# Kernel tuning notes

Measured on AMD Instinct MI355X. Metric: run time of the kernel, lower is better.

Reference implementation:

```python
import jax, jax.numpy as jnp
import numpy as np

N_NODES = 100000
N_EDGES = 1600000
IN_FEATS = 128
HID = 128
OUT_FEATS = 64


def setup_inputs() -> dict:
    key = jax.random.key(0)
    ks = jax.random.split(key, 8)
    node_ids = jnp.arange(N_NODES, dtype=jnp.int64)
    src = jax.random.randint(ks[0], (N_EDGES,), 0, N_NODES, dtype=jnp.int64)
    dst = jax.random.randint(ks[1], (N_EDGES,), 0, N_NODES, dtype=jnp.int64)
    emb = jax.random.normal(ks[2], (N_NODES, IN_FEATS), dtype=jnp.float32)
    W1 = jax.random.normal(ks[3], (IN_FEATS, HID), dtype=jnp.float32) / np.sqrt(IN_FEATS)
    b1 = jnp.zeros((HID,), dtype=jnp.float32)
    W2 = jax.random.normal(ks[4], (HID, OUT_FEATS), dtype=jnp.float32) / np.sqrt(HID)
    b2 = jnp.zeros((OUT_FEATS,), dtype=jnp.float32)
    return {"node_ids": node_ids, "src": src, "dst": dst, "emb": emb,
            "W1": W1, "b1": b1, "W2": W2, "b2": b2}


def _sym_norms(src, dst):
    # DGL GraphConv norm='both': D_out^{-1/2} on source side, D_in^{-1/2} on dest side,
    # degrees clamped to >= 1.
    ones = jnp.ones(src.shape[0], dtype=jnp.float32)
    deg_out = jax.ops.segment_sum(ones, src, num_segments=N_NODES)
    deg_in = jax.ops.segment_sum(ones, dst, num_segments=N_NODES)
    norm_src = jnp.clip(deg_out, 1.0, None) ** -0.5  # [N]
    norm_dst = jnp.clip(deg_in, 1.0, None) ** -0.5   # [N]
    return norm_src, norm_dst


def _spmm(src, dst, h):
    # rst[dst] += h[src]  (sparse adjacency aggregation)
    return jax.ops.segment_sum(h[src], dst, num_segments=N_NODES)


def reference(node_ids, src, dst, emb, W1, b1, W2, b2):
    norm_src, norm_dst = _sym_norms(src, dst)
    h = emb[node_ids]                                   # [N, IN]
    # Layer 1 (IN -> HID, relu): weight applied after aggregation (in <= out)
    h = _spmm(src, dst, h * norm_src[:, None]) * norm_dst[:, None]
    h = jax.nn.relu(h @ W1 + b1)                        # [N, HID]
    # Dropout(0.5) is identity in eval mode.
    # Layer 2 (HID -> OUT): DGL applies weight BEFORE aggregation when in > out
    h = (h @ W2) * norm_src[:, None]                    # [N, OUT]
    h = _spmm(src, dst, h) * norm_dst[:, None] + b2
    return h
```

## Files before the change

### kernel.cpp

```cpp
#include <hip/hip_runtime.h>

#define N_N 100000
#define N_E 1600000
#define SLOTS 48
#define N_PAD 100096

#define BK_SHIFT 9
#define BK_SIZE 512
#define NBKT 196
#define MAXB 10240
#define EPB2 4096
#define NBLK2 ((N_E + EPB2 - 1) / EPB2)
#define EPT 16

#define BINC_BLKS (2 * NBKT)
#define EMB_BLKS 3125
#define W_BLKS 48

typedef unsigned short ushort_t;
typedef unsigned int uint_t;
typedef _Float16 f16x8 __attribute__((ext_vector_type(8)));
typedef float f32x4 __attribute__((ext_vector_type(4)));

__device__ __forceinline__ ushort_t f2h(float f) {
    union { _Float16 h; ushort_t u; } c; c.h = (_Float16)f; return c.u;
}

__device__ __forceinline__ void acc2h(uint_t v, float wv, float& a, float& b) {
    union { uint_t u; _Float16 h[2]; } c; c.u = v;
    a = fmaf((float)c.h[0], wv, a);
    b = fmaf((float)c.h[1], wv, b);
}

__device__ __forceinline__ void addh(uint_t v, float& a, float& b) {
    union { uint_t u; _Float16 h[2]; } c; c.u = v;
    a += (float)c.h[0];
    b += (float)c.h[1];
}

__global__ void __launch_bounds__(256) k_scatter(
        const int* __restrict__ src, const int* __restrict__ dst,
        int* __restrict__ cur_d, int* __restrict__ cur_s,
        uint_t* __restrict__ pe_dst, uint_t* __restrict__ pe_src) {
    __shared__ int hd[NBKT], hs[NBKT], od[NBKT], os_[NBKT];
    int t = threadIdx.x, blk = blockIdx.x;
    for (int i = t; i < NBKT; i += 256) { hd[i] = 0; hs[i] = 0; }
    __syncthreads();
    int e0 = blk * EPB2;
    int myS[EPT], myD[EPT];
    uint_t myR[EPT];
#pragma unroll
    for (int i = 0; i < EPT; i++) {
        int e = e0 + t + i * 256;
        if (e < N_E) {
            int s = src[e], d = dst[e];
            myS[i] = s; myD[i] = d;
            uint_t rd = (uint_t)atomicAdd(&hd[d >> BK_SHIFT], 1);
            uint_t rs = (uint_t)atomicAdd(&hs[s >> BK_SHIFT], 1);
            myR[i] = rd | (rs << 16);
        }
    }
    __syncthreads();
    for (int i = t; i < NBKT; i += 256) {
        int c = hd[i]; od[i]  = c ? atomicAdd(&cur_d[i], c) : 0;
        c = hs[i];     os_[i] = c ? atomicAdd(&cur_s[i], c) : 0;
    }
    __syncthreads();
#pragma unroll
    for (int i = 0; i < EPT; i++) {
        int e = e0 + t + i * 256;
        if (e < N_E) {
            int s = myS[i], d = myD[i];
            int rd = od[d >> BK_SHIFT] + (int)(myR[i] & 0xffffu);
            int rs = os_[s >> BK_SHIFT] + (int)(myR[i] >> 16);
            if (rd < MAXB) pe_dst[(size_t)(d >> BK_SHIFT) * MAXB + rd] =
                               (uint_t)s | ((uint_t)(d & 511) << 17);
            if (rs < MAXB) pe_src[(size_t)(s >> BK_SHIFT) * MAXB + rs] = (uint_t)s;
        }
    }
}

__global__ void __launch_bounds__(512) k_binC_prep(
        const uint_t* __restrict__ pe_dst, const uint_t* __restrict__ pe_src,
        const int* __restrict__ cur_d, const int* __restrict__ cur_s,
        int* __restrict__ slots, int* __restrict__ cnt,
        float* __restrict__ nd, float* __restrict__ ns,
        const float* __restrict__ emb, ushort_t* __restrict__ embf,
        const float* __restrict__ W1, const float* __restrict__ W2,
        ushort_t* __restrict__ w1f, ushort_t* __restrict__ w2f) {
    int t = threadIdx.x, bb = blockIdx.x;
    if (bb >= BINC_BLKS) {
        int pb = bb - BINC_BLKS;
        if (pb < EMB_BLKS) {
            int i = pb * 1024 + t;
            const float4* E4 = (const float4*)emb;
            ushort4* O4 = (ushort4*)embf;
            float4 v0 = E4[i], v1 = E4[i + 512];
            ushort4 o0, o1;
            o0.x = f2h(v0.x); o0.y = f2h(v0.y); o0.z = f2h(v0.z); o0.w = f2h(v0.w);
            o1.x = f2h(v1.x); o1.y = f2h(v1.y); o1.z = f2h(v1.z); o1.w = f2h(v1.w);
            O4[i] = o0; O4[i + 512] = o1;
        } else {
            int idx = (pb - EMB_BLKS) * 512 + t;
            int j = idx & 7, l = (idx >> 3) & 63;
            int k = (l >> 4) * 8 + j;
            int n = l & 15;
            if (idx < 16384) {
                int kc = (idx >> 9) & 3, nt = idx >> 11;
                w1f[idx] = f2h(W1[(kc * 32 + k) * 128 + nt * 16 + n]);
            } else {
                int i2 = idx - 16384;
                int kc = (i2 >> 9) & 3, nt = i2 >> 11;
                w2f[i2] = f2h(W2[(kc * 32 + k) * 64 + nt * 16 + n]);
            }
        }
        return;
    }
    __shared__ int lc[BK_SIZE];
    for (int i = t; i < BK_SIZE; i += 512) lc[i] = 0;
    __syncthreads();
    if (bb < NBKT) {
        int b = bb;
        int cb = min(cur_d[b], MAXB);
        int nbase = b << BK_SHIFT;
        const uint_t* pe = pe_dst + (size_t)b * MAXB;
        for (int e = t; e < cb; e += 512) {
            uint_t ed = pe[e];
            int dloc = (int)(ed >> 17);
            int s = (int)(ed & 0x1ffffu);
            int pos = atomicAdd(&lc[dloc], 1);
            if (pos < SLOTS) slots[(size_t)(nbase + dloc) * SLOTS + pos] = s;
        }
        __syncthreads();
        for (int i = t; i < BK_SIZE; i += 512) {
            int n = nbase + i;
            if (n < N_N) {
                int c = lc[i];
                cnt[n] = c;
                nd[n] = 1.0f / sqrtf((float)max(c, 1));
            }
        }
    } else {
        int b = bb - NBKT;
        int cb = min(cur_s[b], MAXB);
        int nbase = b << BK_SHIFT;
        const uint_t* pe = pe_src + (size_t)b * MAXB;
        for (int e = t; e < cb; e += 512)
            atomicAdd(&lc[(int)pe[e] - nbase], 1);
        __syncthreads();
        for (int i = t; i < BK_SIZE; i += 512) {
            int n = nbase + i;
            if (n < N_N) ns[n] = 1.0f / sqrtf((float)max(lc[i], 1));
        }
    }
}

__global__ void __launch_bounds__(256) k_spmm1(
        const int* __restrict__ cnt, const int* __restrict__ slots,
        const ushort_t* __restrict__ embf, const float* __restrict__ ns,
        const float* __restrict__ nd, uint_t* __restrict__ aggf) {
    int wid = (blockIdx.x * 256 + (int)threadIdx.x) >> 6;
    int node = __builtin_amdgcn_readfirstlane(wid);
    if (node >= N_N) return;
    int lane = threadIdx.x & 63;
    const int* row = slots + node * SLOTS;
    int len = min(cnt[node], SLOTS);
    float ax0 = 0.f, ay0 = 0.f, ax1 = 0.f, ay1 = 0.f;
    int e = 0;
    int n8 = len & ~7;
    for (; e < n8; e += 8) {
        int s0 = __builtin_amdgcn_readfirstlane(row[e + 0]);
        int s1 = __builtin_amdgcn_readfirstlane(row[e + 1]);
        int s2 = __builtin_amdgcn_readfirstlane(row[e + 2]);
        int s3 = __builtin_amdgcn_readfirstlane(row[e + 3]);
        int s4 = __builtin_amdgcn_readfirstlane(row[e + 4]);
        int s5 = __builtin_amdgcn_readfirstlane(row[e + 5]);
        int s6 = __builtin_amdgcn_readfirstlane(row[e + 6]);
        int s7 = __builtin_amdgcn_readfirstlane(row[e + 7]);
        float w0 = ns[s0], w1 = ns[s1], w2 = ns[s2], w3 = ns[s3];
        float w4 = ns[s4], w5 = ns[s5], w6 = ns[s6], w7 = ns[s7];
        uint_t v0 = ((const uint_t*)(embf + (size_t)s0 * 128))[lane];
        uint_t v1 = ((const uint_t*)(embf + (size_t)s1 * 128))[lane];
        uint_t v2 = ((const uint_t*)(embf + (size_t)s2 * 128))[lane];
        uint_t v3 = ((const uint_t*)(embf + (size_t)s3 * 128))[lane];
        uint_t v4 = ((const uint_t*)(embf + (size_t)s4 * 128))[lane];
        uint_t v5 = ((const uint_t*)(embf + (size_t)s5 * 128))[lane];
        uint_t v6 = ((const uint_t*)(embf + (size_t)s6 * 128))[lane];
        uint_t v7 = ((const uint_t*)(embf + (size_t)s7 * 128))[lane];
        acc2h(v0, w0, ax0, ay0);
        acc2h(v1, w1, ax1, ay1);
        acc2h(v2, w2, ax0, ay0);
        acc2h(v3, w3, ax1, ay1);
        acc2h(v4, w4, ax0, ay0);
        acc2h(v5, w5, ax1, ay1);
        acc2h(v6, w6, ax0, ay0);
        acc2h(v7, w7, ax1, ay1);
    }
    int n4 = len & ~3;
    for (; e < n4; e += 4) {
        int s0 = __builtin_amdgcn_readfirstlane(row[e + 0]);
        int s1 = __builtin_amdgcn_readfirstlane(row[e + 1]);
        int s2 = __builtin_amdgcn_readfirstlane(row[e + 2]);
        int s3 = __builtin_amdgcn_readfirstlane(row[e + 3]);
        float w0 = ns[s0], w1 = ns[s1], w2 = ns[s2], w3 = ns[s3];
        uint_t v0 = ((const uint_t*)(embf + (size_t)s0 * 128))[lane];
        uint_t v1 = ((const uint_t*)(embf + (size_t)s1 * 128))[lane];
        uint_t v2 = ((const uint_t*)(embf + (size_t)s2 * 128))[lane];
        uint_t v3 = ((const uint_t*)(embf + (size_t)s3 * 128))[lane];
        acc2h(v0, w0, ax0, ay0);
        acc2h(v1, w1, ax1, ay1);
        acc2h(v2, w2, ax0, ay0);
        acc2h(v3, w3, ax1, ay1);
    }
    for (; e < len; ++e) {
        int s = __builtin_amdgcn_readfirstlane(row[e]);
        float w = ns[s];
        uint_t v = ((const uint_t*)(embf + (size_t)s * 128))[lane];
        acc2h(v, w, ax0, ay0);
    }
    float sc = nd[node];
    union { _Float16 h[2]; uint_t u; } p;
    p.h[0] = (_Float16)((ax0 + ax1) * sc);
    p.h[1] = (_Float16)((ay0 + ay1) * sc);
    aggf[(size_t)node * 64 + lane] = p.u;
}

#define HSTH 136
__global__ void __launch_bounds__(256, 2) k_gemm(
        const ushort_t* __restrict__ aggf, const ushort_t* __restrict__ w1f,
        const float* __restrict__ b1, const ushort_t* __restrict__ w2f,
        const float* __restrict__ ns, ushort_t* __restrict__ h2b) {
    __shared__ ushort_t sh[128 * HSTH];
    int t = threadIdx.x;
    int w = t >> 6, l = t & 63;
    int quad = l >> 4, lm = l & 15;
    int nb0 = blockIdx.x * 128;

    f16x8 a[2][4];
#pragma unroll
    for (int rt = 0; rt < 2; rt++)
#pragma unroll
        for (int kc = 0; kc < 4; kc++)
            a[rt][kc] = *(const f16x8*)(aggf
                + (size_t)(nb0 + rt * 64 + w * 16 + lm) * 128 + kc * 32 + quad * 8);

    f32x4 acc[2][8];
#pragma unroll
    for (int rt = 0; rt < 2; rt++)
#pragma unroll
        for (int nt = 0; nt < 8; nt++) acc[rt][nt] = (f32x4){0.f, 0.f, 0.f, 0.f};

#pragma unroll
    for (int kc = 0; kc < 4; kc++) {
        f16x8 bq[8];
#pragma unroll
        for (int nt = 0; nt < 8; nt++)
            bq[nt] = *(const f16x8*)(w1f + (((nt * 4 + kc) * 64 + l) << 3));
#pragma unroll
        for (int nt = 0; nt < 8; nt++) {
            acc[0][nt] = __builtin_amdgcn_mfma_f32_16x16x32_f16(a[0][kc], bq[nt], acc[0][nt], 0, 0, 0);
            acc[1][nt] = __builtin_amdgcn_mfma_f32_16x16x32_f16(a[1][kc], bq[nt], acc[1][nt], 0, 0, 0);
        }
    }
#pragma unroll
    for (int nt = 0; nt < 8; nt++) {
        float bb = b1[nt * 16 + lm];
#pragma unroll
        for (int rt = 0; rt < 2; rt++)
#pragma unroll
            for (int r = 0; r < 4; r++) {
                int row = rt * 64 + w * 16 + quad * 4 + r;
                sh[row * HSTH + nt * 16 + lm] = f2h(fmaxf(acc[rt][nt][r] + bb, 0.f));
            }
    }
    __syncthreads();

    f16x8 h[2][4];
#pragma unroll
    for (int rt = 0; rt < 2; rt++)
#pragma unroll
        for (int kc = 0; kc < 4; kc++)
            h[rt][kc] = *(const f16x8*)(sh + (rt * 64 + w * 16 + lm) * HSTH
                                        + kc * 32 + quad * 8);

    f32x4 acc2[2][4];
#pragma unroll
    for (int rt = 0; rt < 2; rt++)
#pragma unroll
        for (int q = 0; q < 4; q++) acc2[rt][q] = (f32x4){0.f, 0.f, 0.f, 0.f};

#pragma unroll
    for (int kc = 0; kc < 4; kc++) {
        f16x8 b2q[4];
#pragma unroll
        for (int q = 0; q < 4; q++)
            b2q[q] = *(const f16x8*)(w2f + (((q * 4 + kc) * 64 + l) << 3));
#pragma unroll
        for (int q = 0; q < 4; q++) {
            acc2[0][q] = __builtin_amdgcn_mfma_f32_16x16x32_f16(h[0][kc], b2q[q], acc2[0][q], 0, 0, 0);
            acc2[1][q] = __builtin_amdgcn_mfma_f32_16x16x32_f16(h[1][kc], b2q[q], acc2[1][q], 0, 0, 0);
        }
    }
#pragma unroll
    for (int rt = 0; rt < 2; rt++)
#pragma unroll
        for (int r = 0; r < 4; r++) {
            int node = nb0 + rt * 64 + w * 16 + quad * 4 + r;
            if (node < N_N) {
                float s = ns[node];
#pragma unroll
                for (int q = 0; q < 4; q++)
                    h2b[(size_t)node * 64 + q * 16 + lm] = f2h(acc2[rt][q][r] * s);
            }
        }
}

__global__ void __launch_bounds__(256) k_spmm2(
        const int* __restrict__ cnt, const int* __restrict__ slots,
        const ushort_t* __restrict__ h2b, const float* __restrict__ nd,
        const float* __restrict__ b2, float* __restrict__ out) {
    int wid = (blockIdx.x * 256 + (int)threadIdx.x) >> 6;
    int node = __builtin_amdgcn_readfirstlane(wid);
    if (node >= N_N) return;
    int lane = threadIdx.x & 63;
    int half = lane >> 5, w32 = lane & 31;
    const int* row = slots + node * SLOTS;
    int len = min(cnt[node], SLOTS);
    const uint_t* H = (const uint_t*)h2b;
    float a0 = 0.f, a1 = 0.f, b0 = 0.f, b1v = 0.f;
    int e = 0;
    int n8 = len & ~7;
    for (; e < n8; e += 8) {
        int i0 = e + half;
        int s0 = row[i0], s1 = row[i0 + 2], s2 = row[i0 + 4], s3 = row[i0 + 6];
        uint_t v0 = H[(size_t)s0 * 32 + w32];
        uint_t v1 = H[(size_t)s1 * 32 + w32];
        uint_t v2 = H[(size_t)s2 * 32 + w32];
        uint_t v3 = H[(size_t)s3 * 32 + w32];
        addh(v0, a0, a1);
        addh(v1, b0, b1v);
        addh(v2, a0, a1);
        addh(v3, b0, b1v);
    }
    for (; e + 1 < len; e += 2) {
        int s = row[e + half];
        uint_t v = H[(size_t)s * 32 + w32];
        addh(v, a0, a1);
    }
    if (e < len && half == 0) {
        int s = row[e];
        uint_t v = H[(size_t)s * 32 + w32];
        addh(v, a0, a1);
    }
    a0 += b0; a1 += b1v;
    a0 += __shfl_xor(a0, 32);
    a1 += __shfl_xor(a1, 32);
    if (half == 0) {
        float sc = nd[node];
        float2 bb = ((const float2*)b2)[w32];
        float2 o;
        o.x = a0 * sc + bb.x;
        o.y = a1 * sc + bb.y;
        ((float2*)(out + (size_t)node * 64))[w32] = o;
    }
}

extern "C" void kernel_launch(void* const* d_in, const int* in_sizes, int n_in,
                              void* d_out, int out_size, void* d_ws, size_t ws_size,
                              hipStream_t stream) {
    const int* src = (const int*)d_in[1];
    const int* dst = (const int*)d_in[2];
    const float* emb = (const float*)d_in[3];
    const float* W1 = (const float*)d_in[4];
    const float* b1 = (const float*)d_in[5];
    const float* W2 = (const float*)d_in[6];
    const float* b2 = (const float*)d_in[7];
    float* out = (float*)d_out;

    int* cur_d   = (int*)d_ws;
    int* cur_s   = cur_d + 256;
    int* cnt     = cur_s + 256;
    float* ns    = (float*)(cnt + N_PAD);
    float* nd    = ns + N_PAD;
    int* slots   = (int*)(nd + N_PAD);
    uint_t* pe_dst = (uint_t*)(slots + (size_t)N_N * SLOTS);
    uint_t* pe_src = pe_dst + (size_t)NBKT * MAXB;
    ushort_t* embf = (ushort_t*)(pe_src + (size_t)NBKT * MAXB);
    uint_t* aggf = (uint_t*)(embf + (size_t)N_PAD * 128);
    ushort_t* w1f = (ushort_t*)(aggf + (size_t)N_PAD * 64);
    ushort_t* w2f = w1f + 16384;
    ushort_t* h2b = w2f + 8192;

    hipMemsetAsync(cur_d, 0, sizeof(int) * 512, stream);
    k_scatter  <<<NBLK2, 256, 0, stream>>>(src, dst, cur_d, cur_s, pe_dst, pe_src);
    k_binC_prep<<<BINC_BLKS + EMB_BLKS + W_BLKS, 512, 0, stream>>>(
        pe_dst, pe_src, cur_d, cur_s, slots, cnt, nd, ns, emb, embf, W1, W2, w1f, w2f);
    k_spmm1 <<<(N_N + 3) / 4, 256, 0, stream>>>(cnt, slots, embf, ns, nd, aggf);
    k_gemm  <<<N_PAD / 128, 256, 0, stream>>>((const ushort_t*)aggf, w1f, b1, w2f, ns, h2b);
    k_spmm2 <<<(N_N + 3) / 4, 256, 0, stream>>>(cnt, slots, h2b, nd, b2, out);
}
```

Baseline: 299.2 us.

## Count source degrees with global atomics and widen SpMM gathers to 8-byte loads

The source-side degree count no longer goes through a bucketed pe_src scatter plus a second binning pass. It now uses direct global atomicAdds into a per-node counter, which removes a large write and read buffer at the cost of 1.6M global atomics. Both SpMM kernels now split each wavefront across two or four edges at once, with each lane loading uint2 (8 bytes) instead of 4 bytes. Partial sums are combined with cross-lane shuffles, raising memory-level parallelism per wave. The memset grows to clear the per-node counter array.

```diff
diff --git a/kernel.cpp b/kernel.cpp
--- a/kernel.cpp
+++ b/kernel.cpp
@@ -38,32 +38,35 @@
     b += (float)c.h[1];
 }
 
+__device__ __forceinline__ uint_t packh2(float a, float b) {
+    union { _Float16 h[2]; uint_t u; } p;
+    p.h[0] = (_Float16)a; p.h[1] = (_Float16)b;
+    return p.u;
+}
+
 __global__ void __launch_bounds__(256) k_scatter(
         const int* __restrict__ src, const int* __restrict__ dst,
-        int* __restrict__ cur_d, int* __restrict__ cur_s,
-        uint_t* __restrict__ pe_dst, uint_t* __restrict__ pe_src) {
-    __shared__ int hd[NBKT], hs[NBKT], od[NBKT], os_[NBKT];
+        int* __restrict__ cur_d, int* __restrict__ cnt_s,
+        uint_t* __restrict__ pe_dst) {
+    __shared__ int hd[NBKT], od[NBKT];
     int t = threadIdx.x, blk = blockIdx.x;
-    for (int i = t; i < NBKT; i += 256) { hd[i] = 0; hs[i] = 0; }
+    for (int i = t; i < NBKT; i += 256) hd[i] = 0;
     __syncthreads();
     int e0 = blk * EPB2;
-    int myS[EPT], myD[EPT];
-    uint_t myR[EPT];
+    int myS[EPT], myD[EPT], myR[EPT];
 #pragma unroll
     for (int i = 0; i < EPT; i++) {
         int e = e0 + t + i * 256;
         if (e < N_E) {
             int s = src[e], d = dst[e];
             myS[i] = s; myD[i] = d;
-            uint_t rd = (uint_t)atomicAdd(&hd[d >> BK_SHIFT], 1);
-            uint_t rs = (uint_t)atomicAdd(&hs[s >> BK_SHIFT], 1);
-            myR[i] = rd | (rs << 16);
+            myR[i] = atomicAdd(&hd[d >> BK_SHIFT], 1);
+            atomicAdd(&cnt_s[s], 1);
         }
     }
     __syncthreads();
     for (int i = t; i < NBKT; i += 256) {
-        int c = hd[i]; od[i]  = c ? atomicAdd(&cur_d[i], c) : 0;
-        c = hs[i];     os_[i] = c ? atomicAdd(&cur_s[i], c) : 0;
+        int c = hd[i]; od[i] = c ? atomicAdd(&cur_d[i], c) : 0;
     }
     __syncthreads();
 #pragma unroll
@@ -71,18 +74,16 @@
         int e = e0 + t + i * 256;
         if (e < N_E) {
             int s = myS[i], d = myD[i];
-            int rd = od[d >> BK_SHIFT] + (int)(myR[i] & 0xffffu);
-            int rs = os_[s >> BK_SHIFT] + (int)(myR[i] >> 16);
+            int rd = od[d >> BK_SHIFT] + myR[i];
             if (rd < MAXB) pe_dst[(size_t)(d >> BK_SHIFT) * MAXB + rd] =
                                (uint_t)s | ((uint_t)(d & 511) << 17);
-            if (rs < MAXB) pe_src[(size_t)(s >> BK_SHIFT) * MAXB + rs] = (uint_t)s;
         }
     }
 }
 
 __global__ void __launch_bounds__(512) k_binC_prep(
-        const uint_t* __restrict__ pe_dst, const uint_t* __restrict__ pe_src,
-        const int* __restrict__ cur_d, const int* __restrict__ cur_s,
+        const uint_t* __restrict__ pe_dst, const int* __restrict__ cur_d,
+        const int* __restrict__ cnt_s,
         int* __restrict__ slots, int* __restrict__ cnt,
         float* __restrict__ nd, float* __restrict__ ns,
         const float* __restrict__ emb, ushort_t* __restrict__ embf,
@@ -116,41 +117,32 @@
         }
         return;
     }
+    if (bb >= NBKT) {
+        int n = ((bb - NBKT) << BK_SHIFT) + t;
+        if (n < N_N) ns[n] = 1.0f / sqrtf((float)max(cnt_s[n], 1));
+        return;
+    }
     __shared__ int lc[BK_SIZE];
     for (int i = t; i < BK_SIZE; i += 512) lc[i] = 0;
     __syncthreads();
-    if (bb < NBKT) {
-        int b = bb;
-        int cb = min(cur_d[b], MAXB);
-        int nbase = b << BK_SHIFT;
-        const uint_t* pe = pe_dst + (size_t)b * MAXB;
-        for (int e = t; e < cb; e += 512) {
-            uint_t ed = pe[e];
-            int dloc = (int)(ed >> 17);
-            int s = (int)(ed & 0x1ffffu);
-            int pos = atomicAdd(&lc[dloc], 1);
-            if (pos < SLOTS) slots[(size_t)(nbase + dloc) * SLOTS + pos] = s;
-        }
-        __syncthreads();
-        for (int i = t; i < BK_SIZE; i += 512) {
-            int n = nbase + i;
-            if (n < N_N) {
-                int c = lc[i];
-                cnt[n] = c;
-                nd[n] = 1.0f / sqrtf((float)max(c, 1));
-            }
-        }
-    } else {
-        int b = bb - NBKT;
-        int cb = min(cur_s[b], MAXB);
-        int nbase = b << BK_SHIFT;
-        const uint_t* pe = pe_src + (size_t)b * MAXB;
-        for (int e = t; e < cb; e += 512)
-            atomicAdd(&lc[(int)pe[e] - nbase], 1);
-        __syncthreads();
-        for (int i = t; i < BK_SIZE; i += 512) {
-            int n = nbase + i;
-            if (n < N_N) ns[n] = 1.0f / sqrtf((float)max(lc[i], 1));
+    int b = bb;
+    int cb = min(cur_d[b], MAXB);
+    int nbase = b << BK_SHIFT;
+    const uint_t* pe = pe_dst + (size_t)b * MAXB;
+    for (int e = t; e < cb; e += 512) {
+        uint_t ed = pe[e];
+        int dloc = (int)(ed >> 17);
+        int s = (int)(ed & 0x1ffffu);
+        int pos = atomicAdd(&lc[dloc], 1);
+        if (pos < SLOTS) slots[(size_t)(nbase + dloc) * SLOTS + pos] = s;
+    }
+    __syncthreads();
+    for (int i = t; i < BK_SIZE; i += 512) {
+        int n = nbase + i;
+        if (n < N_N) {
+            int c = lc[i];
+            cnt[n] = c;
+            nd[n] = 1.0f / sqrtf((float)max(c, 1));
         }
     }
 }
@@ -163,66 +155,69 @@
     int node = __builtin_amdgcn_readfirstlane(wid);
     if (node >= N_N) return;
     int lane = threadIdx.x & 63;
+    int h = lane >> 5, w32 = lane & 31;
     const int* row = slots + node * SLOTS;
     int len = min(cnt[node], SLOTS);
-    float ax0 = 0.f, ay0 = 0.f, ax1 = 0.f, ay1 = 0.f;
+    const uint2* E2 = (const uint2*)embf;
+    float a0 = 0.f, a1 = 0.f, a2 = 0.f, a3 = 0.f;
     int e = 0;
-    int n8 = len & ~7;
-    for (; e < n8; e += 8) {
-        int s0 = __builtin_amdgcn_readfirstlane(row[e + 0]);
-        int s1 = __builtin_amdgcn_readfirstlane(row[e + 1]);
-        int s2 = __builtin_amdgcn_readfirstlane(row[e + 2]);
-        int s3 = __builtin_amdgcn_readfirstlane(row[e + 3]);
-        int s4 = __builtin_amdgcn_readfirstlane(row[e + 4]);
-        int s5 = __builtin_amdgcn_readfirstlane(row[e + 5]);
-        int s6 = __builtin_amdgcn_readfirstlane(row[e + 6]);
-        int s7 = __builtin_amdgcn_readfirstlane(row[e + 7]);
+    int n16 = len & ~15;
+    for (; e < n16; e += 16) {
+        const int* rp = row + e + h;
+        int s0 = rp[0],  s1 = rp[2],  s2 = rp[4],  s3 = rp[6];
+        int s4 = rp[8],  s5 = rp[10], s6 = rp[12], s7 = rp[14];
         float w0 = ns[s0], w1 = ns[s1], w2 = ns[s2], w3 = ns[s3];
         float w4 = ns[s4], w5 = ns[s5], w6 = ns[s6], w7 = ns[s7];
-        uint_t v0 = ((const uint_t*)(embf + (size_t)s0 * 128))[lane];
-        uint_t v1 = ((const uint_t*)(embf + (size_t)s1 * 128))[lane];
-        uint_t v2 = ((const uint_t*)(embf + (size_t)s2 * 128))[lane];
-        uint_t v3 = ((const uint_t*)(embf + (size_t)s3 * 128))[lane];
-        uint_t v4 = ((const uint_t*)(embf + (size_t)s4 * 128))[lane];
-        uint_t v5 = ((const uint_t*)(embf + (size_t)s5 * 128))[lane];
-        uint_t v6 = ((const uint_t*)(embf + (size_t)s6 * 128))[lane];
-        uint_t v7 = ((const uint_t*)(embf + (size_t)s7 * 128))[lane];
-        acc2h(v0, w0, ax0, ay0);
-        acc2h(v1, w1, ax1, ay1);
-        acc2h(v2, w2, ax0, ay0);
-        acc2h(v3, w3, ax1, ay1);
-        acc2h(v4, w4, ax0, ay0);
-        acc2h(v5, w5, ax1, ay1);
-        acc2h(v6, w6, ax0, ay0);
-        acc2h(v7, w7, ax1, ay1);
+        uint2 v0 = E2[(size_t)s0 * 32 + w32];
+        uint2 v1 = E2[(size_t)s1 * 32 + w32];
+        uint2 v2 = E2[(size_t)s2 * 32 + w32];
+        uint2 v3 = E2[(size_t)s3 * 32 + w32];
+        uint2 v4 = E2[(size_t)s4 * 32 + w32];
+        uint2 v5 = E2[(size_t)s5 * 32 + w32];
+        uint2 v6 = E2[(size_t)s6 * 32 + w32];
+        uint2 v7 = E2[(size_t)s7 * 32 + w32];
+        acc2h(v0.x, w0, a0, a1); acc2h(v0.y, w0, a2, a3);
+        acc2h(v1.x, w1, a0, a1); acc2h(v1.y, w1, a2, a3);
+        acc2h(v2.x, w2, a0, a1); acc2h(v2.y, w2, a2, a3);
+        acc2h(v3.x, w3, a0, a1); acc2h(v3.y, w3, a2, a3);
+        acc2h(v4.x, w4, a0, a1); acc2h(v4.y, w4, a2, a3);
+        acc2h(v5.x, w5, a0, a1); acc2h(v5.y, w5, a2, a3);
+        acc2h(v6.x, w6, a0, a1); acc2h(v6.y, w6, a2, a3);
+        acc2h(v7.x, w7, a0, a1); acc2h(v7.y, w7, a2, a3);
     }
     int n4 = len & ~3;
     for (; e < n4; e += 4) {
-        int s0 = __builtin_amdgcn_readfirstlane(row[e + 0]);
-        int s1 = __builtin_amdgcn_readfirstlane(row[e + 1]);
-        int s2 = __builtin_amdgcn_readfirstlane(row[e + 2]);
-        int s3 = __builtin_amdgcn_readfirstlane(row[e + 3]);
-        float w0 = ns[s0], w1 = ns[s1], w2 = ns[s2], w3 = ns[s3];
-        uint_t v0 = ((const uint_t*)(embf + (size_t)s0 * 128))[lane];
-        uint_t v1 = ((const uint_t*)(embf + (size_t)s1 * 128))[lane];
-        uint_t v2 = ((const uint_t*)(embf + (size_t)s2 * 128))[lane];
-        uint_t v3 = ((const uint_t*)(embf + (size_t)s3 * 128))[lane];
-        acc2h(v0, w0, ax0, ay0);
-        acc2h(v1, w1, ax1, ay1);
-        acc2h(v2, w2, ax0, ay0);
-        acc2h(v3, w3, ax1, ay1);
-    }
-    for (; e < len; ++e) {
-        int s = __builtin_amdgcn_readfirstlane(row[e]);
+        const int* rp = row + e + h;
+        int s0 = rp[0], s1 = rp[2];
+        float w0 = ns[s0], w1 = ns[s1];
+        uint2 v0 = E2[(size_t)s0 * 32 + w32];
+        uint2 v1 = E2[(size_t)s1 * 32 + w32];
+        acc2h(v0.x, w0, a0, a1); acc2h(v0.y, w0, a2, a3);
+        acc2h(v1.x, w1, a0, a1); acc2h(v1.y, w1, a2, a3);
+    }
+    for (; e + 1 < len; e += 2) {
+        int s = row[e + h];
         float w = ns[s];
-        uint_t v = ((const uint_t*)(embf + (size_t)s * 128))[lane];
-        acc2h(v, w, ax0, ay0);
-    }
-    float sc = nd[node];
-    union { _Float16 h[2]; uint_t u; } p;
-    p.h[0] = (_Float16)((ax0 + ax1) * sc);
-    p.h[1] = (_Float16)((ay0 + ay1) * sc);
-    aggf[(size_t)node * 64 + lane] = p.u;
+        uint2 v = E2[(size_t)s * 32 + w32];
+        acc2h(v.x, w, a0, a1); acc2h(v.y, w, a2, a3);
+    }
+    if (e < len && h == 0) {
+        int s = row[e];
+        float w = ns[s];
+        uint2 v = E2[(size_t)s * 32 + w32];
+        acc2h(v.x, w, a0, a1); acc2h(v.y, w, a2, a3);
+    }
+    a0 += __shfl_xor(a0, 32);
+    a1 += __shfl_xor(a1, 32);
+    a2 += __shfl_xor(a2, 32);
+    a3 += __shfl_xor(a3, 32);
+    if (h == 0) {
+        float sc = nd[node];
+        uint2 o;
+        o.x = packh2(a0 * sc, a1 * sc);
+        o.y = packh2(a2 * sc, a3 * sc);
+        ((uint2*)(aggf + (size_t)node * 64))[w32] = o;
+    }
 }
 
 #define HSTH 136
@@ -275,13 +270,13 @@
     }
     __syncthreads();
 
-    f16x8 h[2][4];
+    f16x8 hh[2][4];
 #pragma unroll
     for (int rt = 0; rt < 2; rt++)
 #pragma unroll
         for (int kc = 0; kc < 4; kc++)
-            h[rt][kc] = *(const f16x8*)(sh + (rt * 64 + w * 16 + lm) * HSTH
-                                        + kc * 32 + quad * 8);
+            hh[rt][kc] = *(const f16x8*)(sh + (rt * 64 + w * 16 + lm) * HSTH
+                                         + kc * 32 + quad * 8);
 
     f32x4 acc2[2][4];
 #pragma unroll
@@ -297,8 +292,8 @@
             b2q[q] = *(const f16x8*)(w2f + (((q * 4 + kc) * 64 + l) << 3));
 #pragma unroll
         for (int q = 0; q < 4; q++) {
-            acc2[0][q] = __builtin_amdgcn_mfma_f32_16x16x32_f16(h[0][kc], b2q[q], acc2[0][q], 0, 0, 0);
-            acc2[1][q] = __builtin_amdgcn_mfma_f32_16x16x32_f16(h[1][kc], b2q[q], acc2[1][q], 0, 0, 0);
+            acc2[0][q] = __builtin_amdgcn_mfma_f32_16x16x32_f16(hh[0][kc], b2q[q], acc2[0][q], 0, 0, 0);
+            acc2[1][q] = __builtin_amdgcn_mfma_f32_16x16x32_f16(hh[1][kc], b2q[q], acc2[1][q], 0, 0, 0);
         }
     }
 #pragma unroll
@@ -323,45 +318,49 @@
     int node = __builtin_amdgcn_readfirstlane(wid);
     if (node >= N_N) return;
     int lane = threadIdx.x & 63;
-    int half = lane >> 5, w32 = lane & 31;
+    int q = lane >> 4, w16 = lane & 15;
     const int* row = slots + node * SLOTS;
     int len = min(cnt[node], SLOTS);
-    const uint_t* H = (const uint_t*)h2b;
-    float a0 = 0.f, a1 = 0.f, b0 = 0.f, b1v = 0.f;
+    const uint2* H2 = (const uint2*)h2b;
+    float a0 = 0.f, a1 = 0.f, a2 = 0.f, a3 = 0.f;
     int e = 0;
-    int n8 = len & ~7;
-    for (; e < n8; e += 8) {
-        int i0 = e + half;
-        int s0 = row[i0], s1 = row[i0 + 2], s2 = row[i0 + 4], s3 = row[i0 + 6];
-        uint_t v0 = H[(size_t)s0 * 32 + w32];
-        uint_t v1 = H[(size_t)s1 * 32 + w32];
-        uint_t v2 = H[(size_t)s2 * 32 + w32];
-        uint_t v3 = H[(size_t)s3 * 32 + w32];
-        addh(v0, a0, a1);
-        addh(v1, b0, b1v);
-        addh(v2, a0, a1);
-        addh(v3, b0, b1v);
-    }
-    for (; e + 1 < len; e += 2) {
-        int s = row[e + half];
-        uint_t v = H[(size_t)s * 32 + w32];
-        addh(v, a0, a1);
-    }
-    if (e < len && half == 0) {
-        int s = row[e];
-        uint_t v = H[(size_t)s * 32 + w32];
-        addh(v, a0, a1);
-    }
-    a0 += b0; a1 += b1v;
-    a0 += __shfl_xor(a0, 32);
-    a1 += __shfl_xor(a1, 32);
-    if (half == 0) {
+    int n16 = len & ~15;
+    for (; e < n16; e += 16) {
+        const int* rp = row + e + q;
+        int s0 = rp[0], s1 = rp[4], s2 = rp[8], s3 = rp[12];
+        uint2 v0 = H2[(size_t)s0 * 16 + w16];
+        uint2 v1 = H2[(size_t)s1 * 16 + w16];
+        uint2 v2 = H2[(size_t)s2 * 16 + w16];
+        uint2 v3 = H2[(size_t)s3 * 16 + w16];
+        addh(v0.x, a0, a1); addh(v0.y, a2, a3);
+        addh(v1.x, a0, a1); addh(v1.y, a2, a3);
+        addh(v2.x, a0, a1); addh(v2.y, a2, a3);
+        addh(v3.x, a0, a1); addh(v3.y, a2, a3);
+    }
+    int n4 = len & ~3;
+    for (; e < n4; e += 4) {
+        int s = row[e + q];
+        uint2 v = H2[(size_t)s * 16 + w16];
+        addh(v.x, a0, a1); addh(v.y, a2, a3);
+    }
+    if (e < len && q < len - e) {
+        int s = row[e + q];
+        uint2 v = H2[(size_t)s * 16 + w16];
+        addh(v.x, a0, a1); addh(v.y, a2, a3);
+    }
+    a0 += __shfl_xor(a0, 16); a1 += __shfl_xor(a1, 16);
+    a2 += __shfl_xor(a2, 16); a3 += __shfl_xor(a3, 16);
+    a0 += __shfl_xor(a0, 32); a1 += __shfl_xor(a1, 32);
+    a2 += __shfl_xor(a2, 32); a3 += __shfl_xor(a3, 32);
+    if (q == 0) {
         float sc = nd[node];
-        float2 bb = ((const float2*)b2)[w32];
-        float2 o;
+        float4 bb = ((const float4*)b2)[w16];
+        float4 o;
         o.x = a0 * sc + bb.x;
         o.y = a1 * sc + bb.y;
-        ((float2*)(out + (size_t)node * 64))[w32] = o;
+        o.z = a2 * sc + bb.z;
+        o.w = a3 * sc + bb.w;
+        ((float4*)(out + (size_t)node * 64))[w16] = o;
     }
 }
 
@@ -378,23 +377,22 @@
     float* out = (float*)d_out;
 
     int* cur_d   = (int*)d_ws;
-    int* cur_s   = cur_d + 256;
-    int* cnt     = cur_s + 256;
+    int* cnt_s   = cur_d + 256;
+    int* cnt     = cnt_s + N_PAD;
     float* ns    = (float*)(cnt + N_PAD);
     float* nd    = ns + N_PAD;
     int* slots   = (int*)(nd + N_PAD);
     uint_t* pe_dst = (uint_t*)(slots + (size_t)N_N * SLOTS);
-    uint_t* pe_src = pe_dst + (size_t)NBKT * MAXB;
-    ushort_t* embf = (ushort_t*)(pe_src + (size_t)NBKT * MAXB);
+    ushort_t* embf = (ushort_t*)(pe_dst + (size_t)NBKT * MAXB);
     uint_t* aggf = (uint_t*)(embf + (size_t)N_PAD * 128);
     ushort_t* w1f = (ushort_t*)(aggf + (size_t)N_PAD * 64);
     ushort_t* w2f = w1f + 16384;
     ushort_t* h2b = w2f + 8192;
 
-    hipMemsetAsync(cur_d, 0, sizeof(int) * 512, stream);
-    k_scatter  <<<NBLK2, 256, 0, stream>>>(src, dst, cur_d, cur_s, pe_dst, pe_src);
+    hipMemsetAsync(cur_d, 0, sizeof(int) * (256 + N_PAD), stream);
+    k_scatter  <<<NBLK2, 256, 0, stream>>>(src, dst, cur_d, cnt_s, pe_dst);
     k_binC_prep<<<BINC_BLKS + EMB_BLKS + W_BLKS, 512, 0, stream>>>(
-        pe_dst, pe_src, cur_d, cur_s, slots, cnt, nd, ns, emb, embf, W1, W2, w1f, w2f);
+        pe_dst, cur_d, cnt_s, slots, cnt, nd, ns, emb, embf, W1, W2, w1f, w2f);
     k_spmm1 <<<(N_N + 3) / 4, 256, 0, stream>>>(cnt, slots, embf, ns, nd, aggf);
     k_gemm  <<<N_PAD / 128, 256, 0, stream>>>((const ushort_t*)aggf, w1f, b1, w2f, ns, h2b);
     k_spmm2 <<<(N_N + 3) / 4, 256, 0, stream>>>(cnt, slots, h2b, nd, b2, out);
```

New measurement: 337.0 us. 1.13x slower.

## Move fp16 conversion into scatter kernel and widen spmm2 loads

Applied to the files above, without the earlier changes.

The emb and weight fp16 conversion blocks move out of the bucket-binning kernel and into the edge-scatter kernel, which now handles half as many edges per block and so launches more blocks. The conversion then runs alongside the scatter, and the binning kernel is left with only the edge work. The second SpMM now has four edges processed in parallel per wavefront, with 8-byte loads per lane, and reduces the partial sums with two shuffle stages. The aim is to overlap the independent conversion with the scatter and to get more memory parallelism in the gather. The cost is more shuffle reductions in the SpMM and a larger grid in the scatter kernel.

```diff
diff --git a/kernel.cpp b/kernel.cpp
--- a/kernel.cpp
+++ b/kernel.cpp
@@ -9,13 +9,12 @@
 #define BK_SIZE 512
 #define NBKT 196
 #define MAXB 10240
-#define EPB2 4096
+#define EPB2 2048
 #define NBLK2 ((N_E + EPB2 - 1) / EPB2)
-#define EPT 16
-
-#define BINC_BLKS (2 * NBKT)
-#define EMB_BLKS 3125
-#define W_BLKS 48
+#define EPT 8
+
+#define EMBB 6250
+#define WB 96
 
 typedef unsigned short ushort_t;
 typedef unsigned int uint_t;
@@ -38,70 +37,33 @@
     b += (float)c.h[1];
 }
 
-__global__ void __launch_bounds__(256) k_scatter(
+__device__ __forceinline__ uint_t packh2(float a, float b) {
+    union { _Float16 h[2]; uint_t u; } p;
+    p.h[0] = (_Float16)a; p.h[1] = (_Float16)b;
+    return p.u;
+}
+
+__global__ void __launch_bounds__(256) k_scatter_prep(
         const int* __restrict__ src, const int* __restrict__ dst,
         int* __restrict__ cur_d, int* __restrict__ cur_s,
-        uint_t* __restrict__ pe_dst, uint_t* __restrict__ pe_src) {
-    __shared__ int hd[NBKT], hs[NBKT], od[NBKT], os_[NBKT];
-    int t = threadIdx.x, blk = blockIdx.x;
-    for (int i = t; i < NBKT; i += 256) { hd[i] = 0; hs[i] = 0; }
-    __syncthreads();
-    int e0 = blk * EPB2;
-    int myS[EPT], myD[EPT];
-    uint_t myR[EPT];
-#pragma unroll
-    for (int i = 0; i < EPT; i++) {
-        int e = e0 + t + i * 256;
-        if (e < N_E) {
-            int s = src[e], d = dst[e];
-            myS[i] = s; myD[i] = d;
-            uint_t rd = (uint_t)atomicAdd(&hd[d >> BK_SHIFT], 1);
-            uint_t rs = (uint_t)atomicAdd(&hs[s >> BK_SHIFT], 1);
-            myR[i] = rd | (rs << 16);
-        }
-    }
-    __syncthreads();
-    for (int i = t; i < NBKT; i += 256) {
-        int c = hd[i]; od[i]  = c ? atomicAdd(&cur_d[i], c) : 0;
-        c = hs[i];     os_[i] = c ? atomicAdd(&cur_s[i], c) : 0;
-    }
-    __syncthreads();
-#pragma unroll
-    for (int i = 0; i < EPT; i++) {
-        int e = e0 + t + i * 256;
-        if (e < N_E) {
-            int s = myS[i], d = myD[i];
-            int rd = od[d >> BK_SHIFT] + (int)(myR[i] & 0xffffu);
-            int rs = os_[s >> BK_SHIFT] + (int)(myR[i] >> 16);
-            if (rd < MAXB) pe_dst[(size_t)(d >> BK_SHIFT) * MAXB + rd] =
-                               (uint_t)s | ((uint_t)(d & 511) << 17);
-            if (rs < MAXB) pe_src[(size_t)(s >> BK_SHIFT) * MAXB + rs] = (uint_t)s;
-        }
-    }
-}
-
-__global__ void __launch_bounds__(512) k_binC_prep(
-        const uint_t* __restrict__ pe_dst, const uint_t* __restrict__ pe_src,
-        const int* __restrict__ cur_d, const int* __restrict__ cur_s,
-        int* __restrict__ slots, int* __restrict__ cnt,
-        float* __restrict__ nd, float* __restrict__ ns,
+        uint_t* __restrict__ pe_dst, uint_t* __restrict__ pe_src,
         const float* __restrict__ emb, ushort_t* __restrict__ embf,
         const float* __restrict__ W1, const float* __restrict__ W2,
         ushort_t* __restrict__ w1f, ushort_t* __restrict__ w2f) {
-    int t = threadIdx.x, bb = blockIdx.x;
-    if (bb >= BINC_BLKS) {
-        int pb = bb - BINC_BLKS;
-        if (pb < EMB_BLKS) {
-            int i = pb * 1024 + t;
+    int t = threadIdx.x, blk = blockIdx.x;
+    if (blk >= NBLK2) {
+        int pb = blk - NBLK2;
+        if (pb < EMBB) {
+            int i = pb * 512 + t;
             const float4* E4 = (const float4*)emb;
             ushort4* O4 = (ushort4*)embf;
-            float4 v0 = E4[i], v1 = E4[i + 512];
+            float4 v0 = E4[i], v1 = E4[i + 256];
             ushort4 o0, o1;
             o0.x = f2h(v0.x); o0.y = f2h(v0.y); o0.z = f2h(v0.z); o0.w = f2h(v0.w);
             o1.x = f2h(v1.x); o1.y = f2h(v1.y); o1.z = f2h(v1.z); o1.w = f2h(v1.w);
-            O4[i] = o0; O4[i + 512] = o1;
+            O4[i] = o0; O4[i + 256] = o1;
         } else {
-            int idx = (pb - EMB_BLKS) * 512 + t;
+            int idx = (pb - EMBB) * 256 + t;
             int j = idx & 7, l = (idx >> 3) & 63;
             int k = (l >> 4) * 8 + j;
             int n = l & 15;
@@ -116,6 +78,49 @@
         }
         return;
     }
+    __shared__ int hd[NBKT], hs[NBKT], od[NBKT], os_[NBKT];
+    for (int i = t; i < NBKT; i += 256) { hd[i] = 0; hs[i] = 0; }
+    __syncthreads();
+    int e0 = blk * EPB2;
+    int myS[EPT], myD[EPT];
+    uint_t myR[EPT];
+#pragma unroll
+    for (int i = 0; i < EPT; i++) {
+        int e = e0 + t + i * 256;
+        if (e < N_E) {
+            int s = src[e], d = dst[e];
+            myS[i] = s; myD[i] = d;
+            uint_t rd = (uint_t)atomicAdd(&hd[d >> BK_SHIFT], 1);
+            uint_t rs = (uint_t)atomicAdd(&hs[s >> BK_SHIFT], 1);
+            myR[i] = rd | (rs << 16);
+        }
+    }
+    __syncthreads();
+    for (int i = t; i < NBKT; i += 256) {
+        int c = hd[i]; od[i]  = c ? atomicAdd(&cur_d[i], c) : 0;
+        c = hs[i];     os_[i] = c ? atomicAdd(&cur_s[i], c) : 0;
+    }
+    __syncthreads();
+#pragma unroll
+    for (int i = 0; i < EPT; i++) {
+        int e = e0 + t + i * 256;
+        if (e < N_E) {
+            int s = myS[i], d = myD[i];
+            int rd = od[d >> BK_SHIFT] + (int)(myR[i] & 0xffffu);
+            int rs = os_[s >> BK_SHIFT] + (int)(myR[i] >> 16);
+            if (rd < MAXB) pe_dst[(size_t)(d >> BK_SHIFT) * MAXB + rd] =
+                               (uint_t)s | ((uint_t)(d & 511) << 17);
+            if (rs < MAXB) pe_src[(size_t)(s >> BK_SHIFT) * MAXB + rs] = (uint_t)s;
+        }
+    }
+}
+
+__global__ void __launch_bounds__(512) k_binC(
+        const uint_t* __restrict__ pe_dst, const uint_t* __restrict__ pe_src,
+        const int* __restrict__ cur_d, const int* __restrict__ cur_s,
+        int* __restrict__ slots, int* __restrict__ cnt,
+        float* __restrict__ nd, float* __restrict__ ns) {
+    int t = threadIdx.x, bb = blockIdx.x;
     __shared__ int lc[BK_SIZE];
     for (int i = t; i < BK_SIZE; i += 512) lc[i] = 0;
     __syncthreads();
@@ -219,10 +224,7 @@
         acc2h(v, w, ax0, ay0);
     }
     float sc = nd[node];
-    union { _Float16 h[2]; uint_t u; } p;
-    p.h[0] = (_Float16)((ax0 + ax1) * sc);
-    p.h[1] = (_Float16)((ay0 + ay1) * sc);
-    aggf[(size_t)node * 64 + lane] = p.u;
+    aggf[(size_t)node * 64 + lane] = packh2((ax0 + ax1) * sc, (ay0 + ay1) * sc);
 }
 
 #define HSTH 136
@@ -275,13 +277,13 @@
     }
     __syncthreads();
 
-    f16x8 h[2][4];
+    f16x8 hh[2][4];
 #pragma unroll
     for (int rt = 0; rt < 2; rt++)
 #pragma unroll
         for (int kc = 0; kc < 4; kc++)
-            h[rt][kc] = *(const f16x8*)(sh + (rt * 64 + w * 16 + lm) * HSTH
-                                        + kc * 32 + quad * 8);
+            hh[rt][kc] = *(const f16x8*)(sh + (rt * 64 + w * 16 + lm) * HSTH
+                                         + kc * 32 + quad * 8);
 
     f32x4 acc2[2][4];
 #pragma unroll
@@ -297,8 +299,8 @@
             b2q[q] = *(const f16x8*)(w2f + (((q * 4 + kc) * 64 + l) << 3));
 #pragma unroll
         for (int q = 0; q < 4; q++) {
-            acc2[0][q] = __builtin_amdgcn_mfma_f32_16x16x32_f16(h[0][kc], b2q[q], acc2[0][q], 0, 0, 0);
-            acc2[1][q] = __builtin_amdgcn_mfma_f32_16x16x32_f16(h[1][kc], b2q[q], acc2[1][q], 0, 0, 0);
+            acc2[0][q] = __builtin_amdgcn_mfma_f32_16x16x32_f16(hh[0][kc], b2q[q], acc2[0][q], 0, 0, 0);
+            acc2[1][q] = __builtin_amdgcn_mfma_f32_16x16x32_f16(hh[1][kc], b2q[q], acc2[1][q], 0, 0, 0);
         }
     }
 #pragma unroll
@@ -323,45 +325,49 @@
     int node = __builtin_amdgcn_readfirstlane(wid);
     if (node >= N_N) return;
     int lane = threadIdx.x & 63;
-    int half = lane >> 5, w32 = lane & 31;
+    int q = lane >> 4, w16 = lane & 15;
     const int* row = slots + node * SLOTS;
     int len = min(cnt[node], SLOTS);
-    const uint_t* H = (const uint_t*)h2b;
-    float a0 = 0.f, a1 = 0.f, b0 = 0.f, b1v = 0.f;
+    const uint2* H2 = (const uint2*)h2b;
+    float a0 = 0.f, a1 = 0.f, a2 = 0.f, a3 = 0.f;
     int e = 0;
-    int n8 = len & ~7;
-    for (; e < n8; e += 8) {
-        int i0 = e + half;
-        int s0 = row[i0], s1 = row[i0 + 2], s2 = row[i0 + 4], s3 = row[i0 + 6];
-        uint_t v0 = H[(size_t)s0 * 32 + w32];
-        uint_t v1 = H[(size_t)s1 * 32 + w32];
-        uint_t v2 = H[(size_t)s2 * 32 + w32];
-        uint_t v3 = H[(size_t)s3 * 32 + w32];
-        addh(v0, a0, a1);
-        addh(v1, b0, b1v);
-        addh(v2, a0, a1);
-        addh(v3, b0, b1v);
-    }
-    for (; e + 1 < len; e += 2) {
-        int s = row[e + half];
-        uint_t v = H[(size_t)s * 32 + w32];
-        addh(v, a0, a1);
-    }
-    if (e < len && half == 0) {
-        int s = row[e];
-        uint_t v = H[(size_t)s * 32 + w32];
-        addh(v, a0, a1);
-    }
-    a0 += b0; a1 += b1v;
-    a0 += __shfl_xor(a0, 32);
-    a1 += __shfl_xor(a1, 32);
-    if (half == 0) {
+    int n16 = len & ~15;
+    for (; e < n16; e += 16) {
+        const int* rp = row + e + q;
+        int s0 = rp[0], s1 = rp[4], s2 = rp[8], s3 = rp[12];
+        uint2 v0 = H2[(size_t)s0 * 16 + w16];
+        uint2 v1 = H2[(size_t)s1 * 16 + w16];
+        uint2 v2 = H2[(size_t)s2 * 16 + w16];
+        uint2 v3 = H2[(size_t)s3 * 16 + w16];
+        addh(v0.x, a0, a1); addh(v0.y, a2, a3);
+        addh(v1.x, a0, a1); addh(v1.y, a2, a3);
+        addh(v2.x, a0, a1); addh(v2.y, a2, a3);
+        addh(v3.x, a0, a1); addh(v3.y, a2, a3);
+    }
+    int n4 = len & ~3;
+    for (; e < n4; e += 4) {
+        int s = row[e + q];
+        uint2 v = H2[(size_t)s * 16 + w16];
+        addh(v.x, a0, a1); addh(v.y, a2, a3);
+    }
+    if (e < len && q < len - e) {
+        int s = row[e + q];
+        uint2 v = H2[(size_t)s * 16 + w16];
+        addh(v.x, a0, a1); addh(v.y, a2, a3);
+    }
+    a0 += __shfl_xor(a0, 16); a1 += __shfl_xor(a1, 16);
+    a2 += __shfl_xor(a2, 16); a3 += __shfl_xor(a3, 16);
+    a0 += __shfl_xor(a0, 32); a1 += __shfl_xor(a1, 32);
+    a2 += __shfl_xor(a2, 32); a3 += __shfl_xor(a3, 32);
+    if (q == 0) {
         float sc = nd[node];
-        float2 bb = ((const float2*)b2)[w32];
-        float2 o;
+        float4 bb = ((const float4*)b2)[w16];
+        float4 o;
         o.x = a0 * sc + bb.x;
         o.y = a1 * sc + bb.y;
-        ((float2*)(out + (size_t)node * 64))[w32] = o;
+        o.z = a2 * sc + bb.z;
+        o.w = a3 * sc + bb.w;
+        ((float4*)(out + (size_t)node * 64))[w16] = o;
     }
 }
 
@@ -392,9 +398,10 @@
     ushort_t* h2b = w2f + 8192;
 
     hipMemsetAsync(cur_d, 0, sizeof(int) * 512, stream);
-    k_scatter  <<<NBLK2, 256, 0, stream>>>(src, dst, cur_d, cur_s, pe_dst, pe_src);
-    k_binC_prep<<<BINC_BLKS + EMB_BLKS + W_BLKS, 512, 0, stream>>>(
-        pe_dst, pe_src, cur_d, cur_s, slots, cnt, nd, ns, emb, embf, W1, W2, w1f, w2f);
+    k_scatter_prep<<<NBLK2 + EMBB + WB, 256, 0, stream>>>(
+        src, dst, cur_d, cur_s, pe_dst, pe_src, emb, embf, W1, W2, w1f, w2f);
+    k_binC  <<<2 * NBKT, 512, 0, stream>>>(
+        pe_dst, pe_src, cur_d, cur_s, slots, cnt, nd, ns);
     k_spmm1 <<<(N_N + 3) / 4, 256, 0, stream>>>(cnt, slots, embf, ns, nd, aggf);
     k_gemm  <<<N_PAD / 128, 256, 0, stream>>>((const ushort_t*)aggf, w1f, b1, w2f, ns, h2b);
     k_spmm2 <<<(N_N + 3) / 4, 256, 0, stream>>>(cnt, slots, h2b, nd, b2, out);
```

Result: no change. 298.3 us (-0.3%).
